# Kernel tuning notes

Measured on AMD Instinct MI355X. Metric: run time of the kernel, lower is better.

The kernel has to match this reference:

```python
import jax, jax.numpy as jnp
import numpy as np

N_SRC, N_GRID, N_LOCS, K = 2048, 50000, 500, 5
FUDGE = 1.0


def setup_inputs() -> dict:
    key = jax.random.key(0)
    ks = jax.random.split(key, 8)
    # Cartesian coords in meters: x,y in [0, 100 km], depth in [-30 km, 0]
    def coords(k, n, depth_scale):
        xy = jax.random.uniform(k, (n, 2), dtype=jnp.float32) * 100000.0
        z = -jax.random.uniform(jax.random.fold_in(k, 1), (n, 1), dtype=jnp.float32) * depth_scale
        return jnp.concatenate([xy, z], axis=1)
    src = coords(ks[0], N_SRC, 30000.0)
    grid = coords(ks[1], N_GRID, 30000.0)
    locs = coords(ks[2], N_LOCS, 2000.0)  # stations near surface
    ind = jax.random.randint(ks[3], (N_LOCS,), 0, N_LOCS)
    log_amp = jax.random.normal(ks[4], (N_SRC, N_LOCS), dtype=jnp.float32)
    bias = 0.1 * jax.random.normal(ks[5], (N_GRID, N_LOCS, 2), dtype=jnp.float32)
    return {
        "src": src, "ind": ind, "log_amp": log_amp, "phase": 0,
        "locs": locs, "grid": grid,
        "mag_coef": jnp.ones((2,), jnp.float32),
        "epicenter_spatial_coef": -jnp.ones((2,), jnp.float32),
        "depth_spatial_coef": jnp.zeros((2,), jnp.float32),
        "bias": bias,
    }


def reference(src, ind, log_amp, phase, locs, grid, mag_coef,
              epicenter_spatial_coef, depth_spatial_coef, bias):
    # ftrns1 == identity (coords already Cartesian); zvec zeros out depth.
    locs_sel = locs[ind]                                   # [L,3]
    # epicentral (horizontal) pairwise distance, [N,L]
    d0 = jnp.linalg.norm(src[:, None, :2] - locs_sel[None, :, :2], axis=2)
    pw_log_dist_zero = jnp.log10(d0 + FUDGE)
    pw_log_dist_depth = jnp.log10(jnp.abs(src[:, 2][:, None] - locs_sel[:, 2][None, :]) + FUDGE)
    # brute-force kNN of src against grid (in km), via squared distances
    s = src / 1000.0
    g = grid / 1000.0
    d2 = (jnp.sum(s * s, axis=1)[:, None]
          + jnp.sum(g * g, axis=1)[None, :]
          - 2.0 * (s @ g.T))                               # [N,G]
    _, inds = jax.lax.top_k(-d2, K)                        # [N,K]
    bias_sel = bias[:, ind, phase]                         # [G,L]
    b = jnp.mean(bias_sel[inds], axis=1)                   # [N,L]
    denom = jnp.maximum(mag_coef[phase], jnp.float32(1e-12))
    mag = (log_amp
           - epicenter_spatial_coef[phase] * pw_log_dist_zero
           - depth_spatial_coef[phase] * pw_log_dist_depth
           - b) / denom
    return mag
```

## Files before the change

kernel.cpp:

```cpp
#include <hip/hip_runtime.h>
#include <math.h>

#define N_SRC  2048
#define N_GRID 50000
#define N_LOCS 500
#define K_TOP  5
#define SPB    8
#define NCHUNK 8
#define CHUNK  (N_GRID / NCHUNK)
#define CAP    128

typedef unsigned long long u64;

__device__ __forceinline__ u64 pack_key(float d2, int j) {
    unsigned int b = __float_as_uint(d2);
    unsigned int m = (unsigned int)(-(int)(b >> 31)) | 0x80000000u;
    b ^= m;
    return ((u64)b << 32) | (u64)(unsigned int)j;
}

__device__ __forceinline__ float dist2(float sx, float sy, float sz, float s2,
                                       float4 g) {
    float dot = fmaf(sz, g.z, fmaf(sy, g.y, sx * g.x));
    return fmaf(-2.0f, dot, s2 + g.w);
}

__device__ __forceinline__ void vins5(float& a0, float& a1, float& a2,
                                      float& a3, float& a4, float x) {
    bool c3 = x < a3, c2 = x < a2, c1 = x < a1, c0 = x < a0;
    a4 = c3 ? a3 : x;
    a3 = c2 ? a2 : (c3 ? x : a3);
    a2 = c1 ? a1 : (c2 ? x : a2);
    a1 = c0 ? a0 : (c1 ? x : a1);
    a0 = c0 ? x  : a0;
}

__device__ __forceinline__ void kins5(u64& a0, u64& a1, u64& a2,
                                      u64& a3, u64& a4, u64 x) {
    if (x >= a4) return;
    bool c3 = x < a3, c2 = x < a2, c1 = x < a1, c0 = x < a0;
    a4 = c3 ? a3 : x;
    a3 = c2 ? a2 : (c3 ? x : a3);
    a2 = c1 ? a1 : (c2 ? x : a2);
    a1 = c0 ? a0 : (c1 ? x : a1);
    a0 = c0 ? x  : a0;
}

__global__ __launch_bounds__(256) void prep_kernel(
    const float* __restrict__ grid, float4* __restrict__ g4)
{
    int j = blockIdx.x * 256 + threadIdx.x;
    if (j < N_GRID) {
        float gx = grid[(size_t)j*3 + 0] / 1000.0f;
        float gy = grid[(size_t)j*3 + 1] / 1000.0f;
        float gz = grid[(size_t)j*3 + 2] / 1000.0f;
        float g2 = fmaf(gz, gz, fmaf(gy, gy, gx * gx));
        g4[j] = make_float4(gx, gy, gz, g2);
    }
}

__global__ __launch_bounds__(256) void topk_kernel(
    const float* __restrict__ src, const float4* __restrict__ g4,
    u64* __restrict__ part)
{
    __shared__ float minsL[SPB][256];
    __shared__ float TL[SPB];
    __shared__ int   cntL[SPB];
    __shared__ u64   listL[SPB][CAP];

    const int tid   = threadIdx.x;
    const int grp   = blockIdx.x & 255;
    const int chunk = blockIdx.x >> 8;
    const int b0    = grp * SPB;
    const int j0    = chunk * CHUNK;
    const int j1    = j0 + CHUNK;

    float sx[SPB], sy[SPB], sz[SPB], s2[SPB];
    #pragma unroll
    for (int s = 0; s < SPB; ++s) {
        const float* p = src + (size_t)(b0 + s) * 3;
        float x = p[0] / 1000.0f, y = p[1] / 1000.0f, z = p[2] / 1000.0f;
        sx[s] = x; sy[s] = y; sz[s] = z;
        s2[s] = fmaf(z, z, fmaf(y, y, x * x));
    }

    float mn[SPB];
    #pragma unroll
    for (int s = 0; s < SPB; ++s) mn[s] = INFINITY;

    for (int j = j0 + tid; j < j1; j += 256) {
        float4 g = g4[j];
        #pragma unroll
        for (int s = 0; s < SPB; ++s)
            mn[s] = fminf(mn[s], dist2(sx[s], sy[s], sz[s], s2[s], g));
    }
    #pragma unroll
    for (int s = 0; s < SPB; ++s) minsL[s][tid] = mn[s];
    if (tid < SPB) cntL[tid] = 0;
    __syncthreads();

    const int lane = tid & 63;
    const int w    = tid >> 6;
    for (int s = w; s < SPB; s += 4) {
        float a0 = INFINITY, a1 = INFINITY, a2 = INFINITY,
              a3 = INFINITY, a4 = INFINITY;
        #pragma unroll
        for (int q = 0; q < 4; ++q) {
            float x = minsL[s][lane * 4 + q];
            if (x < a4) vins5(a0, a1, a2, a3, a4, x);
        }
        #pragma unroll
        for (int off = 32; off >= 1; off >>= 1) {
            float b0_ = __shfl_down(a0, off), b1_ = __shfl_down(a1, off),
                  b2_ = __shfl_down(a2, off), b3_ = __shfl_down(a3, off),
                  b4_ = __shfl_down(a4, off);
            if (b0_ < a4) vins5(a0, a1, a2, a3, a4, b0_);
            if (b1_ < a4) vins5(a0, a1, a2, a3, a4, b1_);
            if (b2_ < a4) vins5(a0, a1, a2, a3, a4, b2_);
            if (b3_ < a4) vins5(a0, a1, a2, a3, a4, b3_);
            if (b4_ < a4) vins5(a0, a1, a2, a3, a4, b4_);
        }
        if (lane == 0) TL[s] = a4;
    }
    __syncthreads();

    float Ts[SPB];
    #pragma unroll
    for (int s = 0; s < SPB; ++s) Ts[s] = TL[s];

    for (int j = j0 + tid; j < j1; j += 256) {
        float4 g = g4[j];
        #pragma unroll
        for (int s = 0; s < SPB; ++s) {
            float d2 = dist2(sx[s], sy[s], sz[s], s2[s], g);
            if (d2 <= Ts[s]) {
                int p = atomicAdd(&cntL[s], 1);
                if (p < CAP) listL[s][p] = pack_key(d2, j);
            }
        }
    }
    __syncthreads();

    for (int s = w; s < SPB; s += 4) {
        int n = cntL[s]; n = n < CAP ? n : CAP;
        u64 a0 = ~0ull, a1 = ~0ull, a2 = ~0ull, a3 = ~0ull, a4 = ~0ull;
        u64 x0 = (lane      < n) ? listL[s][lane]      : ~0ull;
        u64 x1 = (lane + 64 < n) ? listL[s][lane + 64] : ~0ull;
        kins5(a0, a1, a2, a3, a4, x0);
        kins5(a0, a1, a2, a3, a4, x1);
        #pragma unroll
        for (int off = 32; off >= 1; off >>= 1) {
            u64 b0_ = __shfl_down(a0, off), b1_ = __shfl_down(a1, off),
                b2_ = __shfl_down(a2, off), b3_ = __shfl_down(a3, off),
                b4_ = __shfl_down(a4, off);
            kins5(a0, a1, a2, a3, a4, b0_);
            kins5(a0, a1, a2, a3, a4, b1_);
            kins5(a0, a1, a2, a3, a4, b2_);
            kins5(a0, a1, a2, a3, a4, b3_);
            kins5(a0, a1, a2, a3, a4, b4_);
        }
        if (lane == 0) {
            u64* dst = part + ((size_t)(b0 + s) * NCHUNK + chunk) * K_TOP;
            dst[0] = a0; dst[1] = a1; dst[2] = a2; dst[3] = a3; dst[4] = a4;
        }
    }
}

__global__ __launch_bounds__(256) void merge_kernel(
    const u64* __restrict__ part, int* __restrict__ topk)
{
    int s = blockIdx.x * 256 + threadIdx.x;
    if (s >= N_SRC) return;
    u64 a0 = ~0ull, a1 = ~0ull, a2 = ~0ull, a3 = ~0ull, a4 = ~0ull;
    const u64* p = part + (size_t)s * NCHUNK * K_TOP;
    #pragma unroll
    for (int q = 0; q < NCHUNK * K_TOP; ++q)
        kins5(a0, a1, a2, a3, a4, p[q]);
    int* dst = topk + (size_t)s * K_TOP;
    dst[0] = (int)(a0 & 0xFFFFFFFFu);
    dst[1] = (int)(a1 & 0xFFFFFFFFu);
    dst[2] = (int)(a2 & 0xFFFFFFFFu);
    dst[3] = (int)(a3 & 0xFFFFFFFFu);
    dst[4] = (int)(a4 & 0xFFFFFFFFu);
}

__global__ __launch_bounds__(256) void mag_kernel(
    const float* __restrict__ src, const int* __restrict__ ind,
    const float* __restrict__ log_amp, const int* __restrict__ phase_p,
    const float* __restrict__ locs, const float* __restrict__ mag_coef,
    const float* __restrict__ epc_p, const float* __restrict__ depc_p,
    const float* __restrict__ bias, const int* __restrict__ topk,
    float* __restrict__ out)
{
    __shared__ float ctab[N_LOCS];
    __shared__ int   sind[N_LOCS];

    const int i  = blockIdx.x;
    const int ph = phase_p[0];
    const float denom = fmaxf(mag_coef[ph], 1e-12f);
    const float epc   = epc_p[ph];
    const float depc  = depc_p[ph];

    const float sxv = src[(size_t)i*3 + 0];
    const float syv = src[(size_t)i*3 + 1];
    const float szv = src[(size_t)i*3 + 2];

    const int* tk = topk + (size_t)i * K_TOP;
    const int t0 = tk[0], t1 = tk[1], t2 = tk[2], t3 = tk[3], t4 = tk[4];

    for (int il = threadIdx.x; il < N_LOCS; il += 256) {
        const float lx = locs[(size_t)il*3 + 0];
        const float ly = locs[(size_t)il*3 + 1];
        const float lz = locs[(size_t)il*3 + 2];
        const float dx = sxv - lx, dy = syv - ly;
        const float d0 = sqrtf(fmaf(dy, dy, dx * dx));
        const float pz = log10f(d0 + 1.0f);
        const float pd = log10f(fabsf(szv - lz) + 1.0f);
        const int   col = il * 2 + ph;
        float bsum = bias[(size_t)t0 * (N_LOCS*2) + col]
                   + bias[(size_t)t1 * (N_LOCS*2) + col]
                   + bias[(size_t)t2 * (N_LOCS*2) + col]
                   + bias[(size_t)t3 * (N_LOCS*2) + col]
                   + bias[(size_t)t4 * (N_LOCS*2) + col];
        const float bm = bsum / 5.0f;
        ctab[il] = fmaf(-epc, pz, fmaf(-depc, pd, -bm));
        sind[il] = ind[il];
    }
    __syncthreads();

    for (int l = threadIdx.x; l < N_LOCS; l += 256) {
        const float la = log_amp[(size_t)i * N_LOCS + l];
        out[(size_t)i * N_LOCS + l] = (la + ctab[sind[l]]) / denom;
    }
}

extern "C" void kernel_launch(void* const* d_in, const int* in_sizes, int n_in,
                              void* d_out, int out_size, void* d_ws, size_t ws_size,
                              hipStream_t stream) {
    const float* src      = (const float*)d_in[0];
    const int*   ind      = (const int*)  d_in[1];
    const float* log_amp  = (const float*)d_in[2];
    const int*   phase    = (const int*)  d_in[3];
    const float* locs     = (const float*)d_in[4];
    const float* grid     = (const float*)d_in[5];
    const float* mag_coef = (const float*)d_in[6];
    const float* epc      = (const float*)d_in[7];
    const float* depc     = (const float*)d_in[8];
    const float* bias     = (const float*)d_in[9];
    float* out = (float*)d_out;

    char* ws = (char*)d_ws;
    float4* g4   = (float4*)ws;
    u64*    part = (u64*)(ws + 800000);
    int*    topk = (int*)(ws + 800000 + 655360);

    prep_kernel<<<(N_GRID + 255) / 256, 256, 0, stream>>>(grid, g4);
    topk_kernel<<<(N_SRC / SPB) * NCHUNK, 256, 0, stream>>>(src, g4, part);
    merge_kernel<<<(N_SRC + 255) / 256, 256, 0, stream>>>(part, topk);
    mag_kernel<<<N_SRC, 256, 0, stream>>>(src, ind, log_amp, phase, locs,
                                          mag_coef, epc, depc, bias, topk, out);
}
```

Before: 331.8 us.

## Fuse top-k merge into mag kernel and double grid chunk count

Drops the separate merge kernel. The final merge of per-chunk top-5 candidates now runs at the start of mag_kernel, where one wavefront does it with shuffle reductions and hands the indices to the other threads through shared memory. NCHUNK is raised from 8 to 16, which doubles the number of topk blocks so more of the GPU is busy during the distance scan. In exchange each source has more partial candidates to merge, and the partial buffer grows to 2048*80*8 bytes, which may exceed the space reserved before the old topk offset in the workspace.

```diff
diff --git a/kernel.cpp b/kernel.cpp
--- a/kernel.cpp
+++ b/kernel.cpp
@@ -6,9 +6,10 @@
 #define N_LOCS 500
 #define K_TOP  5
 #define SPB    8
-#define NCHUNK 8
+#define NCHUNK 16
 #define CHUNK  (N_GRID / NCHUNK)
 #define CAP    128
+#define NPART  (NCHUNK * K_TOP)
 
 typedef unsigned long long u64;
 
@@ -166,34 +167,17 @@
     }
 }
 
-__global__ __launch_bounds__(256) void merge_kernel(
-    const u64* __restrict__ part, int* __restrict__ topk)
-{
-    int s = blockIdx.x * 256 + threadIdx.x;
-    if (s >= N_SRC) return;
-    u64 a0 = ~0ull, a1 = ~0ull, a2 = ~0ull, a3 = ~0ull, a4 = ~0ull;
-    const u64* p = part + (size_t)s * NCHUNK * K_TOP;
-    #pragma unroll
-    for (int q = 0; q < NCHUNK * K_TOP; ++q)
-        kins5(a0, a1, a2, a3, a4, p[q]);
-    int* dst = topk + (size_t)s * K_TOP;
-    dst[0] = (int)(a0 & 0xFFFFFFFFu);
-    dst[1] = (int)(a1 & 0xFFFFFFFFu);
-    dst[2] = (int)(a2 & 0xFFFFFFFFu);
-    dst[3] = (int)(a3 & 0xFFFFFFFFu);
-    dst[4] = (int)(a4 & 0xFFFFFFFFu);
-}
-
 __global__ __launch_bounds__(256) void mag_kernel(
     const float* __restrict__ src, const int* __restrict__ ind,
     const float* __restrict__ log_amp, const int* __restrict__ phase_p,
     const float* __restrict__ locs, const float* __restrict__ mag_coef,
     const float* __restrict__ epc_p, const float* __restrict__ depc_p,
-    const float* __restrict__ bias, const int* __restrict__ topk,
+    const float* __restrict__ bias, const u64* __restrict__ part,
     float* __restrict__ out)
 {
     __shared__ float ctab[N_LOCS];
     __shared__ int   sind[N_LOCS];
+    __shared__ int   tsh[K_TOP];
 
     const int i  = blockIdx.x;
     const int ph = phase_p[0];
@@ -201,12 +185,38 @@
     const float epc   = epc_p[ph];
     const float depc  = depc_p[ph];
 
+    if (threadIdx.x < 64) {
+        const int lane = threadIdx.x;
+        const u64* p = part + (size_t)i * NPART;
+        u64 a0 = ~0ull, a1 = ~0ull, a2 = ~0ull, a3 = ~0ull, a4 = ~0ull;
+        kins5(a0, a1, a2, a3, a4, p[lane]);
+        if (lane < NPART - 64) kins5(a0, a1, a2, a3, a4, p[lane + 64]);
+        #pragma unroll
+        for (int off = 32; off >= 1; off >>= 1) {
+            u64 b0_ = __shfl_down(a0, off), b1_ = __shfl_down(a1, off),
+                b2_ = __shfl_down(a2, off), b3_ = __shfl_down(a3, off),
+                b4_ = __shfl_down(a4, off);
+            kins5(a0, a1, a2, a3, a4, b0_);
+            kins5(a0, a1, a2, a3, a4, b1_);
+            kins5(a0, a1, a2, a3, a4, b2_);
+            kins5(a0, a1, a2, a3, a4, b3_);
+            kins5(a0, a1, a2, a3, a4, b4_);
+        }
+        if (lane == 0) {
+            tsh[0] = (int)(a0 & 0xFFFFFFFFu);
+            tsh[1] = (int)(a1 & 0xFFFFFFFFu);
+            tsh[2] = (int)(a2 & 0xFFFFFFFFu);
+            tsh[3] = (int)(a3 & 0xFFFFFFFFu);
+            tsh[4] = (int)(a4 & 0xFFFFFFFFu);
+        }
+    }
+    __syncthreads();
+
+    const int t0 = tsh[0], t1 = tsh[1], t2 = tsh[2], t3 = tsh[3], t4 = tsh[4];
+
     const float sxv = src[(size_t)i*3 + 0];
     const float syv = src[(size_t)i*3 + 1];
     const float szv = src[(size_t)i*3 + 2];
-
-    const int* tk = topk + (size_t)i * K_TOP;
-    const int t0 = tk[0], t1 = tk[1], t2 = tk[2], t3 = tk[3], t4 = tk[4];
 
     for (int il = threadIdx.x; il < N_LOCS; il += 256) {
         const float lx = locs[(size_t)il*3 + 0];
@@ -252,11 +262,9 @@
     char* ws = (char*)d_ws;
     float4* g4   = (float4*)ws;
     u64*    part = (u64*)(ws + 800000);
-    int*    topk = (int*)(ws + 800000 + 655360);
 
     prep_kernel<<<(N_GRID + 255) / 256, 256, 0, stream>>>(grid, g4);
     topk_kernel<<<(N_SRC / SPB) * NCHUNK, 256, 0, stream>>>(src, g4, part);
-    merge_kernel<<<(N_SRC + 255) / 256, 256, 0, stream>>>(part, topk);
     mag_kernel<<<N_SRC, 256, 0, stream>>>(src, ind, log_amp, phase, locs,
-                                          mag_coef, epc, depc, bias, topk, out);
-}
+                                          mag_coef, epc, depc, bias, part, out);
+}
```

Measured after the change: 340.1 us. 1.03x slower.
